# Kernel tuning notes

Hardware: AMD Instinct MI355X
Metric: run time of the kernel (lower is better)

Reference implementation:

```python
import jax, jax.numpy as jnp
import numpy as np

# Model dims
T0 = 2048      # tokens (batch*seq flattened)
D = 2048       # hidden_size
E = 256        # n_routed_experts
K = 8          # num_experts_per_tok
G = 8          # expert groups
EG = 32        # experts per group
R = 64         # tucker rank
I = 1408       # moe_intermediate_size


def setup_inputs() -> dict:
    key = jax.random.key(0)
    ks = jax.random.split(key, 12)
    f = lambda k, s: jax.random.normal(k, s, dtype=jnp.float32) * 0.02
    return {
        "hidden_states": jax.random.normal(ks[0], (T0, D), dtype=jnp.float32),
        "w_gate": f(ks[1], (D, E)),
        # Tucker factors per group: shared in-factor A, per-expert core C, shared out-factor B
        "A_gate": f(ks[2], (G, D, R)), "C_gate": f(ks[3], (G, EG, R, R)), "B_gate": f(ks[4], (G, R, I)),
        "A_up":   f(ks[5], (G, D, R)), "C_up":   f(ks[6], (G, EG, R, R)), "B_up":   f(ks[7], (G, R, I)),
        "A_down": f(ks[8], (G, I, R)), "C_down": f(ks[9], (G, EG, R, R)), "B_down": f(ks[10], (G, R, D)),
    }


def _tucker(x, A, C, B, inner):
    # x: [T, d_in], A: [d_in, R], C: [EG, R, R] gathered per-token, B: [R, d_out]
    h1 = x @ A                                    # [T, R]
    h2 = jnp.einsum('tr,trs->ts', h1, C[inner])   # per-token expert core
    return h2 @ B                                 # [T, d_out]


def reference(hidden_states, w_gate, A_gate, C_gate, B_gate,
              A_up, C_up, B_up, A_down, C_down, B_down):
    # Router: softmax in fp32, top-k, renormalize
    logits = hidden_states @ w_gate                              # [T0, E]
    probs = jax.nn.softmax(logits.astype(jnp.float32), axis=-1)
    rw, sel = jax.lax.top_k(probs, K)                            # [T0, K]
    rw = (rw / rw.sum(axis=-1, keepdims=True)).astype(hidden_states.dtype)

    idx = sel.reshape(-1)          # [T0*K] expert ids of dispatched rows
    gid = idx // EG                # group id
    inner = idx % EG               # expert within group
    x = jnp.repeat(hidden_states, K, axis=0)   # repeat_interleave dispatch [T0*K, D]

    out = jnp.zeros_like(x)
    for g in range(G):             # static loop over 8 structurally distinct groups
        m = (gid == g)[:, None]
        xg = jnp.where(m, x, 0.0)  # masked dispatch (zeros flow to zero through the MLP)
        go = _tucker(xg, A_gate[g], C_gate[g], B_gate[g], inner)
        uo = _tucker(xg, A_up[g],   C_up[g],   B_up[g],   inner)
        inter = jax.nn.silu(go) * uo
        do = _tucker(inter, A_down[g], C_down[g], B_down[g], inner)
        out = out + jnp.where(m, do, 0.0)

    # weighted combine
    return (out.reshape(T0, K, D) * rw[..., None]).sum(axis=1)
```

## Files before the change

kernel.cpp:

```cpp
#include <hip/hip_runtime.h>
#include <math.h>

constexpr int T0n = 2048;
constexpr int Dn  = 2048;
constexpr int En  = 256;
constexpr int Gn  = 8;
constexpr int EGn = 32;
constexpr int Rn  = 64;
constexpr int In  = 1408;

constexpr int NROWS = T0n * 8;
constexpr int SEGCAP = NROWS;
constexpr int KSPLIT = 8;

typedef __attribute__((ext_vector_type(8))) short s8v;
typedef __attribute__((ext_vector_type(4))) float f4v;
#define MFMA16(a, b, c) __builtin_amdgcn_mfma_f32_16x16x32_bf16(a, b, c, 0, 0, 0)

__device__ __forceinline__ unsigned short f2bf(float x) {
  unsigned int u = __float_as_uint(x);
  unsigned int r = (u + 0x7FFFu + ((u >> 16) & 1u)) >> 16;
  return (unsigned short)r;
}

struct TD { const float* src; unsigned short* dst; int rows, cols, nbx, per_batch, base; };
struct TD9 { TD t[9]; };

__global__ __launch_bounds__(256) void k_tcvt9(TD9 D) {
  __shared__ float tbuf[32][33];
  int id = blockIdx.x;
  int ti = 0;
#pragma unroll
  for (int i = 1; i < 9; ++i) ti = (id >= D.t[i].base) ? i : ti;
  TD d = D.t[ti];
  int local = id - d.base;
  int bz = local / d.per_batch;
  int rem = local - bz * d.per_batch;
  int by = rem / d.nbx;
  int bx = rem - by * d.nbx;

  size_t boff = (size_t)bz * d.rows * d.cols;
  const float* src = d.src + boff;
  unsigned short* dst = d.dst + boff;
  int c0 = bx * 32, r0 = by * 32;
  int tx = threadIdx.x & 31, ty = threadIdx.x >> 5;
  for (int i = ty; i < 32; i += 8)
    tbuf[i][tx] = src[(size_t)(r0 + i) * d.cols + c0 + tx];
  __syncthreads();
  for (int i = ty; i < 32; i += 8)
    dst[(size_t)(c0 + i) * d.rows + r0 + tx] = f2bf(tbuf[tx][i]);
}

__global__ __launch_bounds__(256) void k_router_part(
    const float* __restrict__ A, const float* __restrict__ B,
    double* __restrict__ part) {
  __shared__ float As[32][68];
  __shared__ float Bs[32][68];
  const int m0 = blockIdx.y * 64, n0 = blockIdx.x * 64;
  const int kc = blockIdx.z;
  const int kbeg = kc * (Dn / KSPLIT);
  const int tid = threadIdx.x;
  const int ty = tid >> 4, tx = tid & 15;
  const int lm = tid & 63, lk8 = (tid >> 6) * 8;
  const int br = tid >> 3, bc = (tid & 7) * 8;

  double acc[4][4] = {};

  for (int k0 = kbeg; k0 < kbeg + Dn / KSPLIT; k0 += 32) {
    float4 a0 = *(const float4*)&A[(size_t)(m0 + lm) * Dn + k0 + lk8];
    float4 a1 = *(const float4*)&A[(size_t)(m0 + lm) * Dn + k0 + lk8 + 4];
    As[lk8 + 0][lm] = a0.x; As[lk8 + 1][lm] = a0.y;
    As[lk8 + 2][lm] = a0.z; As[lk8 + 3][lm] = a0.w;
    As[lk8 + 4][lm] = a1.x; As[lk8 + 5][lm] = a1.y;
    As[lk8 + 6][lm] = a1.z; As[lk8 + 7][lm] = a1.w;
    *(float4*)&Bs[br][bc]     = *(const float4*)&B[(size_t)(k0 + br) * En + n0 + bc];
    *(float4*)&Bs[br][bc + 4] = *(const float4*)&B[(size_t)(k0 + br) * En + n0 + bc + 4];
    __syncthreads();
#pragma unroll
    for (int kk = 0; kk < 32; ++kk) {
      float4 af = *(const float4*)&As[kk][ty * 4];
      float4 bf = *(const float4*)&Bs[kk][tx * 4];
      double a[4] = {(double)af.x, (double)af.y, (double)af.z, (double)af.w};
      double b[4] = {(double)bf.x, (double)bf.y, (double)bf.z, (double)bf.w};
#pragma unroll
      for (int i = 0; i < 4; ++i)
#pragma unroll
        for (int j = 0; j < 4; ++j)
          acc[i][j] += a[i] * b[j];
    }
    __syncthreads();
  }
  double* prow = part + (size_t)kc * T0n * En;
#pragma unroll
  for (int i = 0; i < 4; ++i) {
    int row = m0 + ty * 4 + i;
#pragma unroll
    for (int j2 = 0; j2 < 2; ++j2) {
      double2 dv;
      dv.x = acc[i][j2 * 2 + 0];
      dv.y = acc[i][j2 * 2 + 1];
      *(double2*)&prow[(size_t)row * En + n0 + tx * 4 + j2 * 2] = dv;
    }
  }
}

__global__ __launch_bounds__(256) void k_topk(
    const double* __restrict__ part, int* __restrict__ sel,
    float* __restrict__ rw, int* __restrict__ cnt_e) {
  const int wid = threadIdx.x >> 6, ln = threadIdx.x & 63;
  const int t = blockIdx.x * 4 + wid;

  double v[4];
#pragma unroll
  for (int j = 0; j < 4; ++j) {
    double s = 0.0;
#pragma unroll
    for (int kc = 0; kc < KSPLIT; ++kc)
      s += part[((size_t)kc * T0n + t) * En + ln + 64 * j];
    v[j] = s;
  }

  float topv[8];
  int topi[8];
#pragma unroll
  for (int k = 0; k < 8; ++k) {
    double bv = v[0]; int bi = ln;
#pragma unroll
    for (int j = 1; j < 4; ++j) {
      int cand = ln + 64 * j;
      if (v[j] > bv || (v[j] == bv && cand < bi)) { bv = v[j]; bi = cand; }
    }
#pragma unroll
    for (int off = 32; off > 0; off >>= 1) {
      double ov = __shfl_xor(bv, off);
      int oi = __shfl_xor(bi, off);
      if (ov > bv || (ov == bv && oi < bi)) { bv = ov; bi = oi; }
    }
    topv[k] = (float)bv; topi[k] = bi;
    if ((bi & 63) == ln) v[bi >> 6] = -1e300;
  }

  if (ln < 8) {
    float m = topv[0];
    float ssum = 0.f;
#pragma unroll
    for (int k = 0; k < 8; ++k) ssum += expf(topv[k] - m);
    rw[t * 8 + ln] = expf(topv[ln] - m) / ssum;
    sel[t * 8 + ln] = topi[ln];
    atomicAdd(&cnt_e[topi[ln]], 1);
  }
}

__global__ __launch_bounds__(256) void k_scan(
    const int* __restrict__ cnt_e, int* __restrict__ off_e,
    int* __restrict__ cur_e, int* __restrict__ grp_n) {
  __shared__ int c[256];
  int tid = threadIdx.x;
  c[tid] = cnt_e[tid];
  __syncthreads();
  int g = tid >> 5, ei = tid & 31;
  int run = 0;
  for (int i = 0; i < ei; ++i) run += c[(g << 5) + i];
  off_e[tid] = g * SEGCAP + run;
  cur_e[tid] = g * SEGCAP + run;
  if (ei == 31) grp_n[g] = run + c[tid];
}

__global__ void k_scatter(const int* __restrict__ sel, int* __restrict__ cur_e,
                          int* __restrict__ rseg) {
  int i = blockIdx.x * 256 + threadIdx.x;
  int e = sel[i];
  int pos = atomicAdd(&cur_e[e], 1);
  rseg[pos] = i;
}

__global__ __launch_bounds__(512) void k_h1_mfma(
    const float* __restrict__ H,
    const unsigned short* __restrict__ AgT, const unsigned short* __restrict__ AuT,
    unsigned short* __restrict__ h1gb, unsigned short* __restrict__ h1ub) {
  const int t0 = blockIdx.x * 64;
  const int g = blockIdx.y;
  const unsigned short* Wg = AgT + (size_t)g * Rn * Dn;
  const unsigned short* Wu = AuT + (size_t)g * Rn * Dn;

  __shared__ unsigned short As[64 * 72];
  __shared__ unsigned short Bg_l[64 * 72];
  __shared__ unsigned short Bu_l[64 * 72];
  const int tid = threadIdx.x;
  const int w = tid >> 6, ln = tid & 63;
  const int path = w >> 2, ws = w & 3;
  const int quad = ln >> 4, lane16 = ln & 15;
  const int j = tid >> 3, q = (tid & 7) * 8;

  f4v S[4] = {};

  for (int k0 = 0; k0 < Dn; k0 += 64) {
    {
      float4 v0 = *(const float4*)&H[(size_t)(t0 + j) * Dn + k0 + q];
      float4 v1 = *(const float4*)&H[(size_t)(t0 + j) * Dn + k0 + q + 4];
      ushort4 o0, o1;
      o0.x = f2bf(v0.x); o0.y = f2bf(v0.y); o0.z = f2bf(v0.z); o0.w = f2bf(v0.w);
      o1.x = f2bf(v1.x); o1.y = f2bf(v1.y); o1.z = f2bf(v1.z); o1.w = f2bf(v1.w);
      *(ushort4*)&As[j * 72 + q] = o0;
      *(ushort4*)&As[j * 72 + q + 4] = o1;
      *(uint4*)&Bg_l[j * 72 + q] = *(const uint4*)&Wg[(size_t)j * Dn + k0 + q];
      *(uint4*)&Bu_l[j * 72 + q] = *(const uint4*)&Wu[(size_t)j * Dn + k0 + q];
    }
    __syncthreads();
    const unsigned short* Bl = path ? Bu_l : Bg_l;
#pragma unroll
    for (int kk = 0; kk < 2; ++kk) {
      s8v a = *(const s8v*)&As[(ws * 16 + lane16) * 72 + kk * 32 + quad * 8];
#pragma unroll
      for (int nt = 0; nt < 4; ++nt) {
        s8v b = *(const s8v*)&Bl[(nt * 16 + lane16) * 72 + kk * 32 + quad * 8];
        S[nt] = MFMA16(a, b, S[nt]);
      }
    }
    __syncthreads();
  }
  unsigned short* out = path ? h1ub : h1gb;
#pragma unroll
  for (int nt = 0; nt < 4; ++nt)
#pragma unroll
    for (int r = 0; r < 4; ++r) {
      int row = t0 + ws * 16 + quad * 4 + r;
      int col = g * 64 + nt * 16 + lane16;
      out[(size_t)row * (Gn * Rn) + col] = f2bf(S[nt][r]);
    }
}

__global__ __launch_bounds__(512) void k_core_gu(
    const unsigned short* __restrict__ h1gb, const unsigned short* __restrict__ h1ub,
    const unsigned short* __restrict__ CgT, const unsigned short* __restrict__ CuT,
    const int* __restrict__ rseg, const int* __restrict__ off_e,
    const int* __restrict__ cnt_e,
    unsigned short* __restrict__ h2gb, unsigned short* __restrict__ h2ub) {
  const int e = blockIdx.x;
  const int ne = cnt_e[e];
  if (ne == 0) return;
  const int g = e >> 5;
  const int base = off_e[e];
  __shared__ unsigned short Cg_l[64 * 72];
  __shared__ unsigned short Cu_l[64 * 72];
  __shared__ unsigned short Ags[64 * 72];
  __shared__ unsigned short Aus[64 * 72];
  __shared__ int rids[64];
  const int tid = threadIdx.x;
  const int w = tid >> 6, ln = tid & 63;
  const int path = w >> 2, ws = w & 3;
  const int quad = ln >> 4, lane16 = ln & 15;
  const int j = tid >> 3, q = (tid & 7) * 8;
  {
    const unsigned short* cg = CgT + (size_t)e * (Rn * Rn);
    const unsigned short* cu = CuT + (size_t)e * (Rn * Rn);
    *(uint4*)&Cg_l[j * 72 + q] = *(const uint4*)&cg[j * 64 + q];
    *(uint4*)&Cu_l[j * 72 + q] = *(const uint4*)&cu[j * 64 + q];
  }
  const int ntile = (ne + 63) >> 6;
  for (int it = 0; it < ntile; ++it) {
    int mi = it * 64 + j;
    int rid = (mi < ne) ? rseg[base + mi] : -1;
    if ((tid & 7) == 0) rids[j] = rid;
    uint4 zg = {0, 0, 0, 0}, zu = {0, 0, 0, 0};
    if (rid >= 0) {
      zg = *(const uint4*)&h1gb[(size_t)(rid >> 3) * (Gn * Rn) + g * 64 + q];
      zu = *(const uint4*)&h1ub[(size_t)(rid >> 3) * (Gn * Rn) + g * 64 + q];
    }
    *(uint4*)&Ags[j * 72 + q] = zg;
    *(uint4*)&Aus[j * 72 + q] = zu;
    __syncthreads();
    const unsigned short* Al = path ? Aus : Ags;
    const unsigned short* Cl = path ? Cu_l : Cg_l;
    f4v S[4] = {};
#pragma unroll
    for (int kk = 0; kk < 2; ++kk) {
      s8v a = *(const s8v*)&Al[(ws * 16 + lane16) * 72 + kk * 32 + quad * 8];
#pragma unroll
      for (int nt = 0; nt < 4; ++nt) {
        s8v b = *(const s8v*)&Cl[(nt * 16 + lane16) * 72 + kk * 32 + quad * 8];
        S[nt] = MFMA16(a, b, S[nt]);
      }
    }
    unsigned short* out = path ? h2ub : h2gb;
#pragma unroll
    for (int nt = 0; nt < 4; ++nt)
#pragma unroll
      for (int r = 0; r < 4; ++r) {
        int rid2 = rids[ws * 16 + quad * 4 + r];
        if (rid2 >= 0)
          out[(size_t)rid2 * 64 + nt * 16 + lane16] = f2bf(S[nt][r]);
      }
    __syncthreads();
  }
}

__global__ __launch_bounds__(256) void k_expand_mfma(
    const unsigned short* __restrict__ h2gb, const unsigned short* __restrict__ h2ub,
    const unsigned short* __restrict__ BgT, const unsigned short* __restrict__ BuT,
    const unsigned short* __restrict__ AdT,
    const int* __restrict__ rseg, const int* __restrict__ grp_n,
    float* __restrict__ h1d) {
  const int g = blockIdx.z;
  const int ng = grp_n[g];
  const int m0 = blockIdx.y * 128;
  if (m0 >= ng) return;
  const int c_beg = blockIdx.x * 6;
  const int c_end = min(22, c_beg + 6);

  __shared__ unsigned short Hg_l[128 * 72];
  __shared__ unsigned short Hu_l[128 * 72];
  __shared__ unsigned short Bg_l[64 * 72];
  __shared__ unsigned short Bu_l[64 * 72];
  __shared__ unsigned short Ad_l[64 * 72];
  __shared__ int rids[128];

  const int tid = threadIdx.x;
  const int w = tid >> 6, ln = tid & 63;
  const int quad = ln >> 4, lane16 = ln & 15;

  if (tid < 128) rids[tid] = (m0 + tid < ng) ? rseg[g * SEGCAP + m0 + tid] : -1;
  __syncthreads();
#pragma unroll
  for (int i = 0; i < 4; ++i) {
    int c = tid + i * 256;
    int row = c >> 3, cc = (c & 7) * 8;
    int rid = rids[row];
    uint4 zg = {0, 0, 0, 0}, zu = {0, 0, 0, 0};
    if (rid >= 0) {
      zg = *(const uint4*)&h2gb[(size_t)rid * 64 + cc];
      zu = *(const uint4*)&h2ub[(size_t)rid * 64 + cc];
    }
    *(uint4*)&Hg_l[row * 72 + cc] = zg;
    *(uint4*)&Hu_l[row * 72 + cc] = zu;
  }

  const unsigned short* Bg_base = BgT + (size_t)g * In * Rn;
  const unsigned short* Bu_base = BuT + (size_t)g * In * Rn;
  const unsigned short* Ad_base = AdT + (size_t)g * Rn * In;

  f4v P[2][4] = {};

  for (int c = c_beg; c < c_end; ++c) {
    const int i0 = c * 64;
#pragma unroll
    for (int i = 0; i < 2; ++i) {
      int cq = tid + i * 256;
      int row = cq >> 3, co = (cq & 7) * 8;
      *(uint4*)&Bg_l[row * 72 + co] = *(const uint4*)&Bg_base[(size_t)(i0 + row) * Rn + co];
      *(uint4*)&Bu_l[row * 72 + co] = *(const uint4*)&Bu_base[(size_t)(i0 + row) * Rn + co];
      *(uint4*)&Ad_l[row * 72 + co] = *(const uint4*)&Ad_base[(size_t)row * In + i0 + co];
    }
    __syncthreads();

    f4v Sg[2][4] = {}, Su[2][4] = {};
#pragma unroll
    for (int kk = 0; kk < 2; ++kk) {
      s8v ag[2], au[2], bg[4], bu[4];
#pragma unroll
      for (int mt = 0; mt < 2; ++mt) {
        ag[mt] = *(const s8v*)&Hg_l[(w * 32 + mt * 16 + lane16) * 72 + kk * 32 + quad * 8];
        au[mt] = *(const s8v*)&Hu_l[(w * 32 + mt * 16 + lane16) * 72 + kk * 32 + quad * 8];
      }
#pragma unroll
      for (int nt = 0; nt < 4; ++nt) {
        bg[nt] = *(const s8v*)&Bg_l[(nt * 16 + lane16) * 72 + kk * 32 + quad * 8];
        bu[nt] = *(const s8v*)&Bu_l[(nt * 16 + lane16) * 72 + kk * 32 + quad * 8];
      }
#pragma unroll
      for (int mt = 0; mt < 2; ++mt)
#pragma unroll
        for (int nt = 0; nt < 4; ++nt) {
          Sg[mt][nt] = MFMA16(ag[mt], bg[nt], Sg[mt][nt]);
          Su[mt][nt] = MFMA16(au[mt], bu[nt], Su[mt][nt]);
        }
    }
    __syncthreads();
    {
      unsigned short* ibuf = (w < 2) ? Bg_l : Bu_l;
#pragma unroll
      for (int mt = 0; mt < 2; ++mt)
#pragma unroll
        for (int nt = 0; nt < 4; ++nt)
#pragma unroll
          for (int r = 0; r < 4; ++r) {
            float sg = Sg[mt][nt][r];
            float v = sg / (1.f + __expf(-sg)) * Su[mt][nt][r];
            int row = (w * 32 + mt * 16 + quad * 4 + r) & 63;
            ibuf[row * 72 + nt * 16 + lane16] = f2bf(v);
          }
    }
    __syncthreads();
#pragma unroll
    for (int kk = 0; kk < 2; ++kk) {
      s8v ai[2], bd[4];
#pragma unroll
      for (int mt = 0; mt < 2; ++mt) {
        const unsigned short* src = (w < 2) ? Bg_l : Bu_l;
        int arow = (w * 32 + mt * 16 + lane16) & 63;
        ai[mt] = *(const s8v*)&src[arow * 72 + kk * 32 + quad * 8];
      }
#pragma unroll
      for (int nt = 0; nt < 4; ++nt)
        bd[nt] = *(const s8v*)&Ad_l[(nt * 16 + lane16) * 72 + kk * 32 + quad * 8];
#pragma unroll
      for (int mt = 0; mt < 2; ++mt)
#pragma unroll
        for (int nt = 0; nt < 4; ++nt)
          P[mt][nt] = MFMA16(ai[mt], bd[nt], P[mt][nt]);
    }
    __syncthreads();
  }

#pragma unroll
  for (int mt = 0; mt < 2; ++mt)
#pragma unroll
    for (int nt = 0; nt < 4; ++nt)
#pragma unroll
      for (int r = 0; r < 4; ++r) {
        int lrow = w * 32 + mt * 16 + quad * 4 + r;
        int rid = rids[lrow];
        if (rid >= 0)
          atomicAdd(&h1d[(size_t)rid * 64 + nt * 16 + lane16], P[mt][nt][r]);
      }
}

__global__ __launch_bounds__(512) void k_core_down(
    const float* __restrict__ h1d, const unsigned short* __restrict__ CdT,
    const float* __restrict__ rw,
    const int* __restrict__ rseg, const int* __restrict__ off_e,
    const int* __restrict__ cnt_e,
    float* __restrict__ y) {
  const int e = blockIdx.x;
  const int ne = cnt_e[e];
  if (ne == 0) return;
  const int g = e >> 5;
  const int base = off_e[e];
  __shared__ unsigned short Bd_l[64 * 72];
  __shared__ unsigned short Ad_l[128 * 72];
  __shared__ int rids[128];
  const int tid = threadIdx.x;
  const int w = tid >> 6, ln = tid & 63;
  const int quad = ln >> 4, lane16 = ln & 15;
  {
    int j = tid >> 3, q = (tid & 7) * 8;
    const unsigned short* cd = CdT + (size_t)e * (Rn * Rn);
    *(uint4*)&Bd_l[j * 72 + q] = *(const uint4*)&cd[j * 64 + q];
  }
  const int gj = tid >> 2, gq = (tid & 3) * 16;
  const int ntile = (ne + 127) >> 7;
  for (int it = 0; it < ntile; ++it) {
    int mi = it * 128 + gj;
    int rid = (mi < ne) ? rseg[base + mi] : -1;
    if ((tid & 3) == 0) rids[gj] = rid;
#pragma unroll
    for (int i = 0; i < 4; ++i) {
      int kb = gq + i * 4;
      float4 vd = {0.f, 0.f, 0.f, 0.f};
      if (rid >= 0) vd = *(const float4*)&h1d[(size_t)rid * 64 + kb];
      ushort4 od;
      od.x = f2bf(vd.x); od.y = f2bf(vd.y); od.z = f2bf(vd.z); od.w = f2bf(vd.w);
      *(ushort4*)&Ad_l[gj * 72 + kb] = od;
    }
    __syncthreads();
    f4v Sd[4] = {};
#pragma unroll
    for (int kk = 0; kk < 2; ++kk) {
      s8v ad = *(const s8v*)&Ad_l[(w * 16 + lane16) * 72 + kk * 32 + quad * 8];
#pragma unroll
      for (int nt = 0; nt < 4; ++nt) {
        s8v bd = *(const s8v*)&Bd_l[(nt * 16 + lane16) * 72 + kk * 32 + quad * 8];
        Sd[nt] = MFMA16(ad, bd, Sd[nt]);
      }
    }
#pragma unroll
    for (int nt = 0; nt < 4; ++nt)
#pragma unroll
      for (int r = 0; r < 4; ++r) {
        int rid2 = rids[w * 16 + quad * 4 + r];
        if (rid2 >= 0) {
          float wgt = rw[rid2];
          atomicAdd(&y[(size_t)(rid2 >> 3) * (Gn * Rn) + g * 64 + nt * 16 + lane16],
                    wgt * Sd[nt][r]);
        }
      }
    __syncthreads();
  }
}

__global__ __launch_bounds__(256) void k_combine(
    const float* __restrict__ y, const unsigned short* __restrict__ BdT,
    float* __restrict__ outp) {
  const int t0 = blockIdx.y * 128, n0 = blockIdx.x * 128;
  __shared__ unsigned short As[128 * 72];
  __shared__ unsigned short Bs[128 * 72];
  const int tid = threadIdx.x;
  const int w = tid >> 6, ln = tid & 63;
  const int quad = ln >> 4, lane16 = ln & 15;
  const int mbase = (w >> 1) * 64, nbase = (w & 1) * 64;

  f4v acc[4][4] = {};

  for (int k0 = 0; k0 < Gn * Rn; k0 += 64) {
#pragma unroll
    for (int i = 0; i < 8; ++i) {
      int c = tid + i * 256;
      int row = c >> 4, cc = (c & 15) * 4;
      float4 v = *(const float4*)&y[(size_t)(t0 + row) * (Gn * Rn) + k0 + cc];
      ushort4 o;
      o.x = f2bf(v.x); o.y = f2bf(v.y); o.z = f2bf(v.z); o.w = f2bf(v.w);
      *(ushort4*)&As[row * 72 + cc] = o;
    }
#pragma unroll
    for (int i = 0; i < 4; ++i) {
      int c = tid + i * 256;
      int row = c >> 3, cc = (c & 7) * 8;
      *(uint4*)&Bs[row * 72 + cc] = *(const uint4*)&BdT[(size_t)(n0 + row) * (Gn * Rn) + k0 + cc];
    }
    __syncthreads();
#pragma unroll
    for (int kk = 0; kk < 2; ++kk) {
      s8v a[4], b[4];
#pragma unroll
      for (int mt = 0; mt < 4; ++mt)
        a[mt] = *(const s8v*)&As[(mbase + mt * 16 + lane16) * 72 + kk * 32 + quad * 8];
#pragma unroll
      for (int nt = 0; nt < 4; ++nt)
        b[nt] = *(const s8v*)&Bs[(nbase + nt * 16 + lane16) * 72 + kk * 32 + quad * 8];
#pragma unroll
      for (int mt = 0; mt < 4; ++mt)
#pragma unroll
        for (int nt = 0; nt < 4; ++nt)
          acc[mt][nt] = MFMA16(a[mt], b[nt], acc[mt][nt]);
    }
    __syncthreads();
  }
#pragma unroll
  for (int mt = 0; mt < 4; ++mt)
#pragma unroll
    for (int nt = 0; nt < 4; ++nt)
#pragma unroll
      for (int r = 0; r < 4; ++r)
        outp[(size_t)(t0 + mbase + mt * 16 + quad * 4 + r) * Dn +
             n0 + nbase + nt * 16 + lane16] = acc[mt][nt][r];
}

extern "C" void kernel_launch(void* const* d_in, const int* in_sizes, int n_in,
                              void* d_out, int out_size, void* d_ws, size_t ws_size,
                              hipStream_t stream) {
  const float* hidden = (const float*)d_in[0];
  const float* w_gate = (const float*)d_in[1];
  const float* A_gate = (const float*)d_in[2];
  const float* C_gate = (const float*)d_in[3];
  const float* B_gate = (const float*)d_in[4];
  const float* A_up   = (const float*)d_in[5];
  const float* C_up   = (const float*)d_in[6];
  const float* B_up   = (const float*)d_in[7];
  const float* A_down = (const float*)d_in[8];
  const float* C_down = (const float*)d_in[9];
  const float* B_down = (const float*)d_in[10];
  float* out = (float*)d_out;

  char* base = (char*)d_ws;
  double* part = (double*)d_ws;
  size_t o = 0;
  unsigned short* h2gb = (unsigned short*)(base + o); o += (size_t)NROWS * Rn * 2;
  unsigned short* h2ub = (unsigned short*)(base + o); o += (size_t)NROWS * Rn * 2;
  unsigned short* AgT  = (unsigned short*)(base + o); o += (size_t)Gn * Rn * Dn * 2;
  unsigned short* AuT  = (unsigned short*)(base + o); o += (size_t)Gn * Rn * Dn * 2;
  unsigned short* BgT  = (unsigned short*)(base + o); o += (size_t)Gn * In * Rn * 2;
  unsigned short* BuT  = (unsigned short*)(base + o); o += (size_t)Gn * In * Rn * 2;
  unsigned short* AdT  = (unsigned short*)(base + o); o += (size_t)Gn * Rn * In * 2;
  unsigned short* BdT  = (unsigned short*)(base + o); o += (size_t)Dn * Gn * Rn * 2;
  unsigned short* CgT  = (unsigned short*)(base + o); o += (size_t)En * Rn * Rn * 2;
  unsigned short* CuT  = (unsigned short*)(base + o); o += (size_t)En * Rn * Rn * 2;
  unsigned short* CdT  = (unsigned short*)(base + o); o += (size_t)En * Rn * Rn * 2;
  unsigned short* h1gb = (unsigned short*)(base + o); o += (size_t)T0n * Gn * Rn * 2;
  unsigned short* h1ub = (unsigned short*)(base + o); o += (size_t)T0n * Gn * Rn * 2;
  float* h1d = (float*)(base + o); o += (size_t)NROWS * Rn * 4;
  float* y   = (float*)(base + o); o += (size_t)T0n * Gn * Rn * 4;
  float* rwp = (float*)(base + o); o += (size_t)NROWS * 4;
  int* sel   = (int*)(base + o); o += (size_t)NROWS * 4;
  int* rseg  = (int*)(base + o); o += (size_t)Gn * SEGCAP * 4;
  int* cnt_e = (int*)(base + o); o += En * 4;
  int* off_e = (int*)(base + o); o += En * 4;
  int* cur_e = (int*)(base + o); o += En * 4;
  int* grp_n = (int*)(base + o); o += Gn * 4;

  hipMemsetAsync(cnt_e, 0, En * sizeof(int), stream);

  k_router_part<<<dim3(En / 64, T0n / 64, KSPLIT), 256, 0, stream>>>(
      hidden, w_gate, part);
  k_topk<<<T0n / 4, 256, 0, stream>>>(part, sel, rwp, cnt_e);
  k_scan<<<1, 256, 0, stream>>>(cnt_e, off_e, cur_e, grp_n);
  k_scatter<<<NROWS / 256, 256, 0, stream>>>(sel, cur_e, rseg);

  hipMemsetAsync(h1d, 0, (size_t)NROWS * Rn * sizeof(float), stream);
  hipMemsetAsync(y,   0, (size_t)T0n * Gn * Rn * sizeof(float), stream);

  {
    TD9 D;
    D.t[0] = {A_gate, AgT, Dn, Rn, Rn / 32, (Rn / 32) * (Dn / 32), 0};
    D.t[1] = {A_up,   AuT, Dn, Rn, Rn / 32, (Rn / 32) * (Dn / 32), 1024};
    D.t[2] = {B_gate, BgT, Rn, In, In / 32, (In / 32) * (Rn / 32), 2048};
    D.t[3] = {B_up,   BuT, Rn, In, In / 32, (In / 32) * (Rn / 32), 2752};
    D.t[4] = {A_down, AdT, In, Rn, Rn / 32, (Rn / 32) * (In / 32), 3456};
    D.t[5] = {B_down, BdT, Gn * Rn, Dn, Dn / 32, (Dn / 32) * (Gn * Rn / 32), 4160};
    D.t[6] = {C_gate, CgT, Rn, Rn, 2, 4, 5184};
    D.t[7] = {C_up,   CuT, Rn, Rn, 2, 4, 6208};
    D.t[8] = {C_down, CdT, Rn, Rn, 2, 4, 7232};
    k_tcvt9<<<8256, 256, 0, stream>>>(D);
  }

  k_h1_mfma<<<dim3(T0n / 64, Gn), 512, 0, stream>>>(hidden, AgT, AuT, h1gb, h1ub);
  k_core_gu<<<En, 512, 0, stream>>>(h1gb, h1ub, CgT, CuT,
                                    rseg, off_e, cnt_e, h2gb, h2ub);
  k_expand_mfma<<<dim3(4, NROWS / 128, Gn), 256, 0, stream>>>(
      h2gb, h2ub, BgT, BuT, AdT, rseg, grp_n, h1d);
  k_core_down<<<En, 512, 0, stream>>>(h1d, CdT, rwp,
                                      rseg, off_e, cnt_e, y);
  k_combine<<<dim3(Dn / 128, T0n / 128), 256, 0, stream>>>(y, BdT, out);
}
```

Measured before the change: 342.8 us.

## Compute router logits with multi-limb int8 MFMA instead of FP64 FMA

```diff
diff --git a/kernel.cpp b/kernel.cpp
--- a/kernel.cpp
+++ b/kernel.cpp
@@ -11,11 +11,13 @@
 
 constexpr int NROWS = T0n * 8;
 constexpr int SEGCAP = NROWS;
-constexpr int KSPLIT = 8;
+constexpr int KS_R = 4;
 
 typedef __attribute__((ext_vector_type(8))) short s8v;
 typedef __attribute__((ext_vector_type(4))) float f4v;
+typedef __attribute__((ext_vector_type(4))) int i4v;
 #define MFMA16(a, b, c) __builtin_amdgcn_mfma_f32_16x16x32_bf16(a, b, c, 0, 0, 0)
+#define MFMAI8(a, b, c) __builtin_amdgcn_mfma_i32_16x16x64_i8(a, b, c, 0, 0, 0)
 
 __device__ __forceinline__ unsigned short f2bf(float x) {
   unsigned int u = __float_as_uint(x);
@@ -51,61 +53,123 @@
     dst[(size_t)(c0 + i) * d.rows + r0 + tx] = f2bf(tbuf[tx][i]);
 }
 
-__global__ __launch_bounds__(256) void k_router_part(
-    const float* __restrict__ A, const float* __restrict__ B,
-    double* __restrict__ part) {
-  __shared__ float As[32][68];
-  __shared__ float Bs[32][68];
-  const int m0 = blockIdx.y * 64, n0 = blockIdx.x * 64;
+__device__ __forceinline__ int4 limbs4(float v, double sc) {
+  double d = (double)v * sc;
+  d = fmin(fmax(d, -2.0e9), 2.0e9);
+  int x = __double2int_rn(d);
+  int l0 = (int)(signed char)(x & 0xff); x = (x - l0) >> 8;
+  int l1 = (int)(signed char)(x & 0xff); x = (x - l1) >> 8;
+  int l2 = (int)(signed char)(x & 0xff); x = (x - l2) >> 8;
+  return make_int4(l0, l1, l2, x);
+}
+
+__global__ __launch_bounds__(256) void k_quant_h(
+    const float* __restrict__ H, char* __restrict__ hq) {
+  const size_t PL = (size_t)T0n * Dn;
+  size_t i = (size_t)blockIdx.x * 256 + threadIdx.x;
+  float4 v = *(const float4*)&H[i * 4];
+  int4 a = limbs4(v.x, 268435456.0);
+  int4 b = limbs4(v.y, 268435456.0);
+  int4 c = limbs4(v.z, 268435456.0);
+  int4 d = limbs4(v.w, 268435456.0);
+  unsigned int p0 = (a.x & 0xff) | ((b.x & 0xff) << 8) | ((c.x & 0xff) << 16) | ((unsigned)(d.x & 0xff) << 24);
+  unsigned int p1 = (a.y & 0xff) | ((b.y & 0xff) << 8) | ((c.y & 0xff) << 16) | ((unsigned)(d.y & 0xff) << 24);
+  unsigned int p2 = (a.z & 0xff) | ((b.z & 0xff) << 8) | ((c.z & 0xff) << 16) | ((unsigned)(d.z & 0xff) << 24);
+  unsigned int p3 = (a.w & 0xff) | ((b.w & 0xff) << 8) | ((c.w & 0xff) << 16) | ((unsigned)(d.w & 0xff) << 24);
+  *(unsigned int*)&hq[0 * PL + i * 4] = p0;
+  *(unsigned int*)&hq[1 * PL + i * 4] = p1;
+  *(unsigned int*)&hq[2 * PL + i * 4] = p2;
+  *(unsigned int*)&hq[3 * PL + i * 4] = p3;
+}
+
+__global__ __launch_bounds__(256) void k_quant_wT(
+    const float* __restrict__ W, char* __restrict__ wqT) {
+  __shared__ float tb[32][33];
+  const size_t PL = (size_t)En * Dn;
+  int kb = blockIdx.x * 32, nb = blockIdx.y * 32;
+  int tx = threadIdx.x & 31, ty = threadIdx.x >> 5;
+  for (int i = ty; i < 32; i += 8)
+    tb[i][tx] = W[(size_t)(kb + i) * En + nb + tx];
+  __syncthreads();
+  for (int i = ty; i < 32; i += 8) {
+    int4 l = limbs4(tb[tx][i], 8589934592.0);
+    size_t off = (size_t)(nb + i) * Dn + kb + tx;
+    wqT[0 * PL + off] = (char)l.x;
+    wqT[1 * PL + off] = (char)l.y;
+    wqT[2 * PL + off] = (char)l.z;
+    wqT[3 * PL + off] = (char)l.w;
+  }
+}
+
+__global__ __launch_bounds__(256) void k_router_i8(
+    const char* __restrict__ hq, const char* __restrict__ wqT,
+    float* __restrict__ part) {
+  __shared__ __align__(16) char Asl[4][64][80];
+  __shared__ __align__(16) char Bsl[4][64][80];
+  const int n0 = blockIdx.x * 64, m0 = blockIdx.y * 64;
   const int kc = blockIdx.z;
-  const int kbeg = kc * (Dn / KSPLIT);
   const int tid = threadIdx.x;
-  const int ty = tid >> 4, tx = tid & 15;
-  const int lm = tid & 63, lk8 = (tid >> 6) * 8;
-  const int br = tid >> 3, bc = (tid & 7) * 8;
-
-  double acc[4][4] = {};
-
-  for (int k0 = kbeg; k0 < kbeg + Dn / KSPLIT; k0 += 32) {
-    float4 a0 = *(const float4*)&A[(size_t)(m0 + lm) * Dn + k0 + lk8];
-    float4 a1 = *(const float4*)&A[(size_t)(m0 + lm) * Dn + k0 + lk8 + 4];
-    As[lk8 + 0][lm] = a0.x; As[lk8 + 1][lm] = a0.y;
-    As[lk8 + 2][lm] = a0.z; As[lk8 + 3][lm] = a0.w;
-    As[lk8 + 4][lm] = a1.x; As[lk8 + 5][lm] = a1.y;
-    As[lk8 + 6][lm] = a1.z; As[lk8 + 7][lm] = a1.w;
-    *(float4*)&Bs[br][bc]     = *(const float4*)&B[(size_t)(k0 + br) * En + n0 + bc];
-    *(float4*)&Bs[br][bc + 4] = *(const float4*)&B[(size_t)(k0 + br) * En + n0 + bc + 4];
-    __syncthreads();
-#pragma unroll
-    for (int kk = 0; kk < 32; ++kk) {
-      float4 af = *(const float4*)&As[kk][ty * 4];
-      float4 bf = *(const float4*)&Bs[kk][tx * 4];
-      double a[4] = {(double)af.x, (double)af.y, (double)af.z, (double)af.w};
-      double b[4] = {(double)bf.x, (double)bf.y, (double)bf.z, (double)bf.w};
-#pragma unroll
-      for (int i = 0; i < 4; ++i)
-#pragma unroll
-        for (int j = 0; j < 4; ++j)
-          acc[i][j] += a[i] * b[j];
-    }
-    __syncthreads();
-  }
-  double* prow = part + (size_t)kc * T0n * En;
-#pragma unroll
-  for (int i = 0; i < 4; ++i) {
-    int row = m0 + ty * 4 + i;
-#pragma unroll
-    for (int j2 = 0; j2 < 2; ++j2) {
-      double2 dv;
-      dv.x = acc[i][j2 * 2 + 0];
-      dv.y = acc[i][j2 * 2 + 1];
-      *(double2*)&prow[(size_t)row * En + n0 + tx * 4 + j2 * 2] = dv;
-    }
-  }
+  const int w = tid >> 6, ln = tid & 63;
+  const int quad = ln >> 4, lane16 = ln & 15;
+
+  const char* ha = hq + ((size_t)w * T0n + m0 + ln) * Dn;
+  const char* ba = wqT + ((size_t)w * En + n0 + ln) * Dn;
+
+  i4v acc[4][5] = {};
+
+  const int kbeg = kc * (Dn / KS_R);
+  for (int k0 = kbeg; k0 < kbeg + Dn / KS_R; k0 += 64) {
+#pragma unroll
+    for (int q = 0; q < 4; ++q) {
+      *(uint4*)&Asl[w][ln][q * 16] = *(const uint4*)&ha[k0 + q * 16];
+      *(uint4*)&Bsl[w][ln][q * 16] = *(const uint4*)&ba[k0 + q * 16];
+    }
+    __syncthreads();
+    i4v b0 = *(const i4v*)&Bsl[0][w * 16 + lane16][quad * 16];
+    i4v b1 = *(const i4v*)&Bsl[1][w * 16 + lane16][quad * 16];
+    i4v b2 = *(const i4v*)&Bsl[2][w * 16 + lane16][quad * 16];
+    i4v b3 = *(const i4v*)&Bsl[3][w * 16 + lane16][quad * 16];
+#pragma unroll
+    for (int mt = 0; mt < 4; ++mt) {
+      i4v a0 = *(const i4v*)&Asl[0][mt * 16 + lane16][quad * 16];
+      i4v a1 = *(const i4v*)&Asl[1][mt * 16 + lane16][quad * 16];
+      i4v a2 = *(const i4v*)&Asl[2][mt * 16 + lane16][quad * 16];
+      i4v a3 = *(const i4v*)&Asl[3][mt * 16 + lane16][quad * 16];
+      acc[mt][0] = MFMAI8(a0, b2, acc[mt][0]);
+      acc[mt][0] = MFMAI8(a1, b1, acc[mt][0]);
+      acc[mt][0] = MFMAI8(a2, b0, acc[mt][0]);
+      acc[mt][1] = MFMAI8(a0, b3, acc[mt][1]);
+      acc[mt][1] = MFMAI8(a1, b2, acc[mt][1]);
+      acc[mt][1] = MFMAI8(a2, b1, acc[mt][1]);
+      acc[mt][1] = MFMAI8(a3, b0, acc[mt][1]);
+      acc[mt][2] = MFMAI8(a1, b3, acc[mt][2]);
+      acc[mt][2] = MFMAI8(a2, b2, acc[mt][2]);
+      acc[mt][2] = MFMAI8(a3, b1, acc[mt][2]);
+      acc[mt][3] = MFMAI8(a2, b3, acc[mt][3]);
+      acc[mt][3] = MFMAI8(a3, b2, acc[mt][3]);
+      acc[mt][4] = MFMAI8(a3, b3, acc[mt][4]);
+    }
+    __syncthreads();
+  }
+
+  float* prow = part + (size_t)kc * T0n * En;
+#pragma unroll
+  for (int mt = 0; mt < 4; ++mt)
+#pragma unroll
+    for (int r = 0; r < 4; ++r) {
+      int row = m0 + mt * 16 + quad * 4 + r;
+      int col = n0 + w * 16 + lane16;
+      double v = (double)acc[mt][0][r] * 0x1p-45 +
+                 (double)acc[mt][1][r] * 0x1p-37 +
+                 (double)acc[mt][2][r] * 0x1p-29 +
+                 (double)acc[mt][3][r] * 0x1p-21 +
+                 (double)acc[mt][4][r] * 0x1p-13;
+      prow[(size_t)row * En + col] = (float)v;
+    }
 }
 
 __global__ __launch_bounds__(256) void k_topk(
-    const double* __restrict__ part, int* __restrict__ sel,
+    const float* __restrict__ part, int* __restrict__ sel,
     float* __restrict__ rw, int* __restrict__ cnt_e) {
   const int wid = threadIdx.x >> 6, ln = threadIdx.x & 63;
   const int t = blockIdx.x * 4 + wid;
@@ -115,8 +179,8 @@
   for (int j = 0; j < 4; ++j) {
     double s = 0.0;
 #pragma unroll
-    for (int kc = 0; kc < KSPLIT; ++kc)
-      s += part[((size_t)kc * T0n + t) * En + ln + 64 * j];
+    for (int kc = 0; kc < KS_R; ++kc)
+      s += (double)part[((size_t)kc * T0n + t) * En + ln + 64 * j];
     v[j] = s;
   }
 
@@ -562,7 +626,6 @@
   float* out = (float*)d_out;
 
   char* base = (char*)d_ws;
-  double* part = (double*)d_ws;
   size_t o = 0;
   unsigned short* h2gb = (unsigned short*)(base + o); o += (size_t)NROWS * Rn * 2;
   unsigned short* h2ub = (unsigned short*)(base + o); o += (size_t)NROWS * Rn * 2;
@@ -586,11 +649,15 @@
   int* off_e = (int*)(base + o); o += En * 4;
   int* cur_e = (int*)(base + o); o += En * 4;
   int* grp_n = (int*)(base + o); o += Gn * 4;
+  float* part = (float*)base;
+  char* hq  = base + (size_t)KS_R * T0n * En * 4;
+  char* wqT = hq + (size_t)4 * T0n * Dn;
 
   hipMemsetAsync(cnt_e, 0, En * sizeof(int), stream);
 
-  k_router_part<<<dim3(En / 64, T0n / 64, KSPLIT), 256, 0, stream>>>(
-      hidden, w_gate, part);
+  k_quant_h<<<T0n * Dn / 1024, 256, 0, stream>>>(hidden, hq);
+  k_quant_wT<<<dim3(Dn / 32, En / 32), 256, 0, stream>>>(w_gate, wqT);
+  k_router_i8<<<dim3(En / 64, T0n / 64, KS_R), 256, 0, stream>>>(hq, wqT, part);
   k_topk<<<T0n / 4, 256, 0, stream>>>(part, sel, rwp, cnt_e);
   k_scan<<<1, 256, 0, stream>>>(cnt_e, off_e, cur_e, grp_n);
   k_scatter<<<NROWS / 256, 256, 0, stream>>>(sel, cur_e, rseg);
```

Result: faster. 333.4 us (-2.7%).
